# Optimization experiments

Hardware: AMD Instinct MI355X
Metric: run time of the kernel (lower is better)

Reference implementation:

```python
import jax, jax.numpy as jnp
import numpy as np

B, T, D, NH, N, NL, V = 1, 4096, 256, 4, 256, 4, 256
TWO_PI = 2.0 * np.pi
THETA = 2.0 ** 16


def _ln(x):
    # LayerNorm over last dim, no affine, eps=1e-5 (torch default)
    mu = x.mean(-1, keepdims=True)
    var = ((x - mu) ** 2).mean(-1, keepdims=True)
    return (x - mu) * jax.lax.rsqrt(var + 1e-5)


def _rope(phases, v):
    # phases: [T,N] broadcast over [B,nh,T,N]; per-index (interleaved-pair) rotation
    v_rot = jnp.stack((-v[..., 1::2], v[..., ::2]), axis=-1).reshape(v.shape)
    ph = (phases % 1.0) * TWO_PI
    return v * jnp.cos(ph) + v_rot * jnp.sin(ph)


def setup_inputs() -> dict:
    key = jax.random.key(0)
    k0, k1, k2, k3, k4, k5 = jax.random.split(key, 6)
    idx = jax.random.randint(k0, (B, T), 0, V)
    embed = jax.random.normal(k1, (V, D), dtype=jnp.float32) * 0.02
    encoder = jax.random.normal(k2, (NH, D, N), dtype=jnp.float32) * 0.02
    encoder_v = jax.random.normal(k3, (NH, D, N), dtype=jnp.float32) * 0.02
    decoder = jax.random.normal(k4, (NH * N, D), dtype=jnp.float32) * 0.02
    lm_head = jax.random.normal(k5, (D, V), dtype=jnp.float32) * 0.02
    freqs = (1.0 / THETA ** (jnp.arange(N, dtype=jnp.float32) / N)) / TWO_PI  # [N]
    return {"idx": idx, "embed": embed, "encoder": encoder,
            "encoder_v": encoder_v, "decoder": decoder,
            "lm_head": lm_head, "freqs": freqs}


def reference(idx, embed, encoder, encoder_v, decoder, lm_head, freqs):
    r_phases = jnp.arange(T, dtype=jnp.float32)[:, None] * freqs[None, :]  # [T,N]
    x = _ln(embed[idx][:, None])  # [B,1,T,D]
    for _ in range(NL):
        x_sparse = jax.nn.relu(x @ encoder)           # [B,nh,T,N]
        QR = _rope(r_phases, x_sparse)                # [B,nh,T,N]
        scores = jnp.tril(QR @ jnp.swapaxes(QR, -1, -2), k=-1)  # [B,nh,T,T], no softmax
        yKV = _ln(scores @ x)                         # [B,nh,T,D] (V broadcast from [B,1,T,D])
        y_sparse = jax.nn.relu(yKV @ encoder_v)       # [B,nh,T,N]
        xy_sparse = x_sparse * y_sparse               # gated sparse activations
        yMLP = jnp.swapaxes(xy_sparse, 1, 2).reshape(B, 1, T, NH * N) @ decoder  # [B,1,T,D]
        x = _ln(x + _ln(yMLP))
    logits = x.reshape(B, T, D) @ lm_head  # [B,T,V]
    return logits
```

## Files before the change

### kernel.cpp

```cpp
#include <hip/hip_runtime.h>
#include <hip/hip_bf16.h>

#define T   4096
#define D   256
#define NH  4
#define NN  256
#define NL  4
#define VV  256
#define CI  64
#define NC  (T/CI)

typedef short bf16x4 __attribute__((ext_vector_type(4)));
typedef short bf16x8 __attribute__((ext_vector_type(8)));
typedef float f32x4  __attribute__((ext_vector_type(4)));

__device__ __forceinline__ short f2bf(float f) {
    union { float f; unsigned u; } v; v.f = f;
    unsigned r = v.u + 0x7fffu + ((v.u >> 16) & 1u);
    return (short)(r >> 16);
}
__device__ __forceinline__ float bf2f(short s) {
    union { unsigned u; float f; } v; v.u = ((unsigned)(unsigned short)s) << 16;
    return v.f;
}
__device__ __forceinline__ f32x4 mfma16(bf16x8 a, bf16x8 b, f32x4 c) {
    return __builtin_amdgcn_mfma_f32_16x16x32_bf16(a, b, c, 0, 0, 0);
}

__global__ void __launch_bounds__(256) k_wtr(const float* __restrict__ src,
                                             short* __restrict__ dst, int R, int C) {
    int b = blockIdx.z, r0 = blockIdx.x * 16, c0 = blockIdx.y * 16;
    int i = threadIdx.x >> 4, j = threadIdx.x & 15;
    __shared__ float tile[16][17];
    tile[i][j] = src[((size_t)b * R + r0 + i) * C + c0 + j];
    __syncthreads();
    dst[((size_t)b * C + c0 + i) * R + r0 + j] = f2bf(tile[j][i]);
}

__global__ void k_rope(const float* __restrict__ freqs,
                       float* __restrict__ rcos, float* __restrict__ rsin) {
    int t = blockIdx.x, n = threadIdx.x;
    float p = (float)t * freqs[n];
    float fr = p - floorf(p);
    float ang = fr * 6.283185307179586f;
    rcos[(size_t)t * NN + n] = cosf(ang);
    rsin[(size_t)t * NN + n] = sinf(ang);
}

__global__ void __launch_bounds__(256) k_embed(const int* __restrict__ idx,
                                               const float* __restrict__ embed,
                                               short* __restrict__ xT) {
    int t0 = blockIdx.x * 32, tid = threadIdx.x;
    __shared__ float ld[32][257];
    __shared__ int ridx[32];
    __shared__ float mu_s[32], rs_s[32];
    if (tid < 32) ridx[tid] = idx[t0 + tid];
    __syncthreads();
    for (int k = 0; k < 32; k++) ld[k][tid] = embed[(size_t)ridx[k] * D + tid];
    __syncthreads();
    int r = tid >> 3, l8 = tid & 7;
    float s = 0.f, q = 0.f;
    for (int d = l8; d < D; d += 8) { float v = ld[r][d]; s += v; q += v * v; }
#pragma unroll
    for (int m = 1; m < 8; m <<= 1) { s += __shfl_xor(s, m); q += __shfl_xor(q, m); }
    if (l8 == 0) {
        float mu = s * (1.f / D);
        float var = q * (1.f / D) - mu * mu;
        mu_s[r] = mu; rs_s[r] = rsqrtf(fmaxf(var, 0.f) + 1e-5f);
    }
    __syncthreads();
    short vals[32];
#pragma unroll
    for (int rr = 0; rr < 32; rr++) vals[rr] = f2bf((ld[rr][tid] - mu_s[rr]) * rs_s[rr]);
    bf16x8* p = (bf16x8*)(xT + (size_t)tid * T + t0);
#pragma unroll
    for (int u = 0; u < 4; u++) p[u] = *(bf16x8*)&vals[u * 8];
}

__global__ void __launch_bounds__(256) k_tr(const short* __restrict__ src,
                                            short* __restrict__ dst, int R, int C) {
    int z = blockIdx.z;
    int c0 = blockIdx.x * 64, r0 = blockIdx.y * 64;
    int tid = threadIdx.x;
    __shared__ short ld[64][72];
    const short* s = src + (size_t)z * R * C;
    short* d = dst + (size_t)z * R * C;
    {
        int i = tid >> 2, c4 = (tid & 3) * 16;
        const bf16x8* p = (const bf16x8*)(s + (size_t)(r0 + i) * C + c0 + c4);
        bf16x8 v0 = p[0], v1 = p[1];
        int sw = (i & 7) << 3;
        *(bf16x8*)&ld[i][c4 ^ sw] = v0;
        *(bf16x8*)&ld[i][(c4 + 8) ^ sw] = v1;
    }
    __syncthreads();
    {
        int j = tid >> 2, r4 = (tid & 3) * 16;
        short vals[16];
#pragma unroll
        for (int m = 0; m < 16; m++) vals[m] = ld[r4 + m][j ^ ((m & 7) << 3)];
        bf16x8* q = (bf16x8*)(d + (size_t)(c0 + j) * R + r0 + r4);
        q[0] = *(bf16x8*)&vals[0];
        q[1] = *(bf16x8*)&vals[8];
    }
}

__global__ void __launch_bounds__(256) k_encode(const short* __restrict__ x_bf,
                                                const short* __restrict__ encT,
                                                const float* __restrict__ rc,
                                                const float* __restrict__ rs,
                                                short* __restrict__ xs,
                                                short* __restrict__ qr) {
    int h = blockIdx.y, t0 = blockIdx.x * 32;
    int tid = threadIdx.x, w = tid >> 6, l = tid & 63;
    int l15 = l & 15, lk = (l >> 4) * 8, lr4 = (l >> 4) * 4;
    int nstrip = w * 64;
    const short* ebase = encT + ((size_t)h * NN + nstrip + l15) * D + lk;
    const short* xbase = x_bf + (size_t)(t0 + l15) * D + lk;
    f32x4 acc[4][2];
#pragma unroll
    for (int rt = 0; rt < 4; rt++)
#pragma unroll
        for (int tt = 0; tt < 2; tt++) acc[rt][tt] = (f32x4){0.f, 0.f, 0.f, 0.f};
    for (int k0 = 0; k0 < D; k0 += 32) {
        bf16x8 a[4], b[2];
#pragma unroll
        for (int rt = 0; rt < 4; rt++) a[rt] = *(const bf16x8*)(ebase + rt * 16 * D + k0);
#pragma unroll
        for (int tt = 0; tt < 2; tt++) b[tt] = *(const bf16x8*)(xbase + tt * 16 * D + k0);
#pragma unroll
        for (int rt = 0; rt < 4; rt++)
#pragma unroll
            for (int tt = 0; tt < 2; tt++) acc[rt][tt] = mfma16(a[rt], b[tt], acc[rt][tt]);
    }
#pragma unroll
    for (int rt = 0; rt < 4; rt++)
#pragma unroll
        for (int tt = 0; tt < 2; tt++) {
            int t = t0 + tt * 16 + l15;
            int n0 = nstrip + rt * 16 + lr4;
            float v[4], rot[4];
#pragma unroll
            for (int r = 0; r < 4; r++) v[r] = fmaxf(acc[rt][tt][r], 0.f);
            rot[0] = -v[1]; rot[1] = v[0]; rot[2] = -v[3]; rot[3] = v[2];
            bf16x4 xsv;
#pragma unroll
            for (int r = 0; r < 4; r++) xsv[r] = f2bf(v[r]);
            *(bf16x4*)(xs + ((size_t)h * T + t) * NN + n0) = xsv;
            float4 cv = *(const float4*)(rc + (size_t)t * NN + n0);
            float4 sv = *(const float4*)(rs + (size_t)t * NN + n0);
            float cc[4] = {cv.x, cv.y, cv.z, cv.w}, ss[4] = {sv.x, sv.y, sv.z, sv.w};
            bf16x4 qv;
#pragma unroll
            for (int r = 0; r < 4; r++) qv[r] = f2bf(v[r] * cc[r] + rot[r] * ss[r]);
            *(bf16x4*)(qr + ((size_t)h * T + t) * NN + n0) = qv;
        }
}

__global__ void __launch_bounds__(256) k_gram(const short* __restrict__ qrT,
                                              const short* __restrict__ xT,
                                              short* __restrict__ Graw) {
    int h = blockIdx.z, c = blockIdx.y, n0 = blockIdx.x * 64;
    int tid = threadIdx.x, w = tid >> 6, l = tid & 63;
    int l15 = l & 15, lk = (l >> 4) * 8, lr4 = (l >> 4) * 4;
    const short* abase = qrT + ((size_t)h * NN + n0 + w * 16 + l15) * T + c * CI + lk;
    const short* bbase = xT + (size_t)l15 * T + c * CI + lk;
    f32x4 acc[16];
#pragma unroll
    for (int dt = 0; dt < 16; dt++) acc[dt] = (f32x4){0.f, 0.f, 0.f, 0.f};
#pragma unroll
    for (int ki = 0; ki < 2; ki++) {
        int k0 = ki * 32;
        bf16x8 a = *(const bf16x8*)(abase + k0);
#pragma unroll
        for (int dt = 0; dt < 16; dt++) {
            bf16x8 b = *(const bf16x8*)(bbase + (size_t)dt * 16 * T + k0);
            acc[dt] = mfma16(a, b, acc[dt]);
        }
    }
#pragma unroll
    for (int dt = 0; dt < 16; dt++) {
        int d = dt * 16 + l15;
        bf16x4 o;
#pragma unroll
        for (int r = 0; r < 4; r++) o[r] = f2bf(acc[dt][r]);
        *(bf16x4*)(Graw + (((size_t)h * NC + c) * D + d) * NN + n0 + w * 16 + lr4) = o;
    }
}

__global__ void __launch_bounds__(256) k_prefix(const short* __restrict__ Graw,
                                                short* __restrict__ Sp) {
    int pos = (blockIdx.x * 256 + threadIdx.x) * 4;
    int h = pos >> 16;
    int rem = pos & 65535;
    float run[4] = {0.f, 0.f, 0.f, 0.f};
    for (int c = 0; c < NC; c++) {
        size_t ix = ((size_t)h * NC + c) * 65536 + rem;
        bf16x4 g = *(const bf16x4*)(Graw + ix);
        bf16x4 o;
#pragma unroll
        for (int e = 0; e < 4; e++) { o[e] = f2bf(run[e]); run[e] += bf2f(g[e]); }
        *(bf16x4*)(Sp + ix) = o;
    }
}

__global__ void __launch_bounds__(256) k_attn(const short* __restrict__ qr,
                                              const short* __restrict__ xT,
                                              const short* __restrict__ Sp,
                                              const short* __restrict__ encvT,
                                              const short* __restrict__ xs,
                                              short* __restrict__ xy) {
    int h = blockIdx.y, t0 = blockIdx.x * 32;
    int c = t0 >> 6, cl0 = t0 & 63;
    int tid = threadIdx.x, w = tid >> 6, l = tid & 63;
    int l15 = l & 15, lk = (l >> 4) * 8, lr4 = (l >> 4) * 4;
    int ts = w & 1, dh = w >> 1;
    __shared__ short P_lds[32][72];
    __shared__ short ynorm[32 * 256];
    __shared__ float lnb[2][32][2];
    int njt = cl0 ? 4 : 2;
    const short* qa  = qr + ((size_t)h * T + t0 + ts * 16 + l15) * NN + lk;
    const short* qpb = qr + ((size_t)h * T + c * CI + l15) * NN + lk;
    const short* sb  = Sp + (((size_t)h * NC + c) * D + dh * 128 + l15) * NN + lk;
    f32x4 akv[8], ap[4];
#pragma unroll
    for (int dt = 0; dt < 8; dt++) akv[dt] = (f32x4){0.f, 0.f, 0.f, 0.f};
#pragma unroll
    for (int jt = 0; jt < 4; jt++) ap[jt] = (f32x4){0.f, 0.f, 0.f, 0.f};
    for (int k0 = 0; k0 < NN; k0 += 32) {
        bf16x8 a = *(const bf16x8*)(qa + k0);
#pragma unroll
        for (int dt = 0; dt < 8; dt++) {
            bf16x8 bs = *(const bf16x8*)(sb + (size_t)dt * 16 * NN + k0);
            akv[dt] = mfma16(a, bs, akv[dt]);
        }
        if (dh == 0) {
#pragma unroll
            for (int jt = 0; jt < 4; jt++) {
                if (jt < njt) {
                    bf16x8 bp = *(const bf16x8*)(qpb + (size_t)jt * 16 * NN + k0);
                    ap[jt] = mfma16(a, bp, ap[jt]);
                }
            }
        }
    }
    if (dh == 0) {
#pragma unroll
        for (int jt = 0; jt < 4; jt++) {
            if (jt < njt) {
#pragma unroll
                for (int r = 0; r < 4; r++) {
                    int il = ts * 16 + lr4 + r;
                    int jcl = jt * 16 + l15;
                    float pv = (jcl < cl0 + il) ? ap[jt][r] : 0.f;
                    P_lds[il][jcl] = f2bf(pv);
                }
            }
        }
    }
    __syncthreads();
    int nks = cl0 ? 2 : 1;
    for (int ki = 0; ki < nks; ki++) {
        int k0 = ki * 32;
        bf16x8 a = *(const bf16x8*)(&P_lds[ts * 16 + l15][k0 + lk]);
#pragma unroll
        for (int dt = 0; dt < 8; dt++) {
            bf16x8 b = *(const bf16x8*)(xT + (size_t)(dh * 128 + dt * 16 + l15) * T + c * CI + k0 + lk);
            akv[dt] = mfma16(a, b, akv[dt]);
        }
    }
    float s[4], q[4], mu[4], rstd[4];
#pragma unroll
    for (int r = 0; r < 4; r++) { s[r] = 0.f; q[r] = 0.f; }
#pragma unroll
    for (int dt = 0; dt < 8; dt++)
#pragma unroll
        for (int r = 0; r < 4; r++) { float v = akv[dt][r]; s[r] += v; q[r] += v * v; }
#pragma unroll
    for (int m = 1; m < 16; m <<= 1)
#pragma unroll
        for (int r = 0; r < 4; r++) { s[r] += __shfl_xor(s[r], m); q[r] += __shfl_xor(q[r], m); }
    if (l15 == 0) {
#pragma unroll
        for (int r = 0; r < 4; r++) {
            int rl = ts * 16 + lr4 + r;
            lnb[dh][rl][0] = s[r]; lnb[dh][rl][1] = q[r];
        }
    }
    __syncthreads();
#pragma unroll
    for (int r = 0; r < 4; r++) {
        int rl = ts * 16 + lr4 + r;
        float st = lnb[0][rl][0] + lnb[1][rl][0];
        float qt = lnb[0][rl][1] + lnb[1][rl][1];
        float m_ = st * (1.f / D);
        float var = qt * (1.f / D) - m_ * m_;
        mu[r] = m_; rstd[r] = rsqrtf(fmaxf(var, 0.f) + 1e-5f);
    }
#pragma unroll
    for (int dt = 0; dt < 8; dt++)
#pragma unroll
        for (int r = 0; r < 4; r++) {
            int row = ts * 16 + lr4 + r;
            int dcol = dh * 128 + dt * 16 + l15;
            ynorm[row * 256 + (dcol ^ ((row & 7) << 3))] = f2bf((akv[dt][r] - mu[r]) * rstd[r]);
        }
    __syncthreads();
    int nstrip = w * 64;
    f32x4 a2[4][2];
#pragma unroll
    for (int nt = 0; nt < 4; nt++)
#pragma unroll
        for (int tt = 0; tt < 2; tt++) a2[nt][tt] = (f32x4){0.f, 0.f, 0.f, 0.f};
    const short* ev = encvT + ((size_t)h * NN + nstrip + l15) * D + lk;
    for (int k0 = 0; k0 < D; k0 += 32) {
        bf16x8 av[4], bv[2];
#pragma unroll
        for (int nt = 0; nt < 4; nt++) av[nt] = *(const bf16x8*)(ev + nt * 16 * D + k0);
#pragma unroll
        for (int tt = 0; tt < 2; tt++) {
            int row = tt * 16 + l15;
            int col = k0 + lk;
            bv[tt] = *(const bf16x8*)&ynorm[row * 256 + (col ^ ((row & 7) << 3))];
        }
#pragma unroll
        for (int nt = 0; nt < 4; nt++)
#pragma unroll
            for (int tt = 0; tt < 2; tt++) a2[nt][tt] = mfma16(av[nt], bv[tt], a2[nt][tt]);
    }
#pragma unroll
    for (int nt = 0; nt < 4; nt++)
#pragma unroll
        for (int tt = 0; tt < 2; tt++) {
            int n0 = nstrip + nt * 16 + lr4;
            int t = t0 + tt * 16 + l15;
            bf16x4 g = *(const bf16x4*)(xs + ((size_t)h * T + t) * NN + n0);
            bf16x4 o;
#pragma unroll
            for (int r = 0; r < 4; r++) o[r] = f2bf(fmaxf(a2[nt][tt][r], 0.f) * bf2f(g[r]));
            *(bf16x4*)(xy + (size_t)t * (NH * NN) + h * NN + n0) = o;
        }
}

__global__ void __launch_bounds__(256) k_mlp(const short* __restrict__ xy,
                                             const short* __restrict__ decT,
                                             short* __restrict__ xT) {
    int t0 = blockIdx.x * 16;
    int tid = threadIdx.x, w = tid >> 6, l = tid & 63;
    int l15 = l & 15, lk = (l >> 4) * 8, lr4 = (l >> 4) * 4;
    __shared__ float lnb[4][16][2];
    const short* abase = xy + (size_t)(t0 + l15) * (NH * NN) + lk;
    const short* bbase = decT + (size_t)(w * 64 + l15) * (NH * NN) + lk;
    f32x4 acc[4];
#pragma unroll
    for (int dt = 0; dt < 4; dt++) acc[dt] = (f32x4){0.f, 0.f, 0.f, 0.f};
    for (int k0 = 0; k0 < NH * NN; k0 += 32) {
        bf16x8 a = *(const bf16x8*)(abase + k0);
#pragma unroll
        for (int dt = 0; dt < 4; dt++) {
            bf16x8 b = *(const bf16x8*)(bbase + (size_t)dt * 16 * (NH * NN) + k0);
            acc[dt] = mfma16(a, b, acc[dt]);
        }
    }
    float s[4], q[4];
#pragma unroll
    for (int r = 0; r < 4; r++) { s[r] = 0.f; q[r] = 0.f; }
#pragma unroll
    for (int dt = 0; dt < 4; dt++)
#pragma unroll
        for (int r = 0; r < 4; r++) { float v = acc[dt][r]; s[r] += v; q[r] += v * v; }
#pragma unroll
    for (int m = 1; m < 16; m <<= 1)
#pragma unroll
        for (int r = 0; r < 4; r++) { s[r] += __shfl_xor(s[r], m); q[r] += __shfl_xor(q[r], m); }
    if (l15 == 0)
#pragma unroll
        for (int r = 0; r < 4; r++) { lnb[w][lr4 + r][0] = s[r]; lnb[w][lr4 + r][1] = q[r]; }
    __syncthreads();
    float mu1[4], rstd1[4];
#pragma unroll
    for (int r = 0; r < 4; r++) {
        float st = 0.f, qt = 0.f;
#pragma unroll
        for (int ww = 0; ww < 4; ww++) { st += lnb[ww][lr4 + r][0]; qt += lnb[ww][lr4 + r][1]; }
        float m_ = st * (1.f / D);
        float var = qt * (1.f / D) - m_ * m_;
        mu1[r] = m_; rstd1[r] = rsqrtf(fmaxf(var, 0.f) + 1e-5f);
    }
    float z[4][4];
#pragma unroll
    for (int dt = 0; dt < 4; dt++) {
        bf16x4 xo = *(const bf16x4*)(xT + (size_t)(w * 64 + dt * 16 + l15) * T + t0 + lr4);
#pragma unroll
        for (int r = 0; r < 4; r++)
            z[dt][r] = bf2f(xo[r]) + (acc[dt][r] - mu1[r]) * rstd1[r];
    }
#pragma unroll
    for (int r = 0; r < 4; r++) { s[r] = 0.f; q[r] = 0.f; }
#pragma unroll
    for (int dt = 0; dt < 4; dt++)
#pragma unroll
        for (int r = 0; r < 4; r++) { float v = z[dt][r]; s[r] += v; q[r] += v * v; }
#pragma unroll
    for (int m = 1; m < 16; m <<= 1)
#pragma unroll
        for (int r = 0; r < 4; r++) { s[r] += __shfl_xor(s[r], m); q[r] += __shfl_xor(q[r], m); }
    __syncthreads();
    if (l15 == 0)
#pragma unroll
        for (int r = 0; r < 4; r++) { lnb[w][lr4 + r][0] = s[r]; lnb[w][lr4 + r][1] = q[r]; }
    __syncthreads();
#pragma unroll
    for (int r = 0; r < 4; r++) {
        float st = 0.f, qt = 0.f;
#pragma unroll
        for (int ww = 0; ww < 4; ww++) { st += lnb[ww][lr4 + r][0]; qt += lnb[ww][lr4 + r][1]; }
        float m_ = st * (1.f / D);
        float var = qt * (1.f / D) - m_ * m_;
        mu1[r] = m_; rstd1[r] = rsqrtf(fmaxf(var, 0.f) + 1e-5f);
    }
#pragma unroll
    for (int dt = 0; dt < 4; dt++) {
        bf16x4 o;
#pragma unroll
        for (int r = 0; r < 4; r++) o[r] = f2bf((z[dt][r] - mu1[r]) * rstd1[r]);
        *(bf16x4*)(xT + (size_t)(w * 64 + dt * 16 + l15) * T + t0 + lr4) = o;
    }
}

__global__ void __launch_bounds__(256) k_logits(const short* __restrict__ x_bf,
                                                const short* __restrict__ lmhT,
                                                float* __restrict__ out) {
    int t0 = blockIdx.x * 16;
    int tid = threadIdx.x, w = tid >> 6, l = tid & 63;
    int l15 = l & 15, lk = (l >> 4) * 8, lr4 = (l >> 4) * 4;
    const short* ab = lmhT + (size_t)(w * 64 + l15) * D + lk;
    const short* bb = x_bf + (size_t)(t0 + l15) * D + lk;
    f32x4 acc[4];
#pragma unroll
    for (int vt = 0; vt < 4; vt++) acc[vt] = (f32x4){0.f, 0.f, 0.f, 0.f};
    for (int k0 = 0; k0 < D; k0 += 32) {
        bf16x8 b = *(const bf16x8*)(bb + k0);
#pragma unroll
        for (int vt = 0; vt < 4; vt++) {
            bf16x8 a = *(const bf16x8*)(ab + (size_t)vt * 16 * D + k0);
            acc[vt] = mfma16(a, b, acc[vt]);
        }
    }
#pragma unroll
    for (int vt = 0; vt < 4; vt++) {
        int t = t0 + l15;
        int v0 = w * 64 + vt * 16 + lr4;
        *(f32x4*)(out + (size_t)t * VV + v0) = acc[vt];
    }
}

extern "C" void kernel_launch(void* const* d_in, const int* in_sizes, int n_in,
                              void* d_out, int out_size, void* d_ws, size_t ws_size,
                              hipStream_t stream) {
    const int*   idx   = (const int*)d_in[0];
    const float* embed = (const float*)d_in[1];
    const float* enc   = (const float*)d_in[2];
    const float* encv  = (const float*)d_in[3];
    const float* dec   = (const float*)d_in[4];
    const float* lmh   = (const float*)d_in[5];
    const float* freqs = (const float*)d_in[6];
    float* out = (float*)d_out;

    float* rc = (float*)d_ws;
    float* rs = rc + (size_t)T * NN;
    short* xT    = (short*)(rs + (size_t)T * NN);
    short* x_bf  = xT + (size_t)D * T;
    short* xs    = x_bf + (size_t)T * D;
    short* qr    = xs + (size_t)NH * T * NN;
    short* qrT   = qr + (size_t)NH * T * NN;
    short* xy    = qrT + (size_t)NH * NN * T;
    short* Graw  = xy + (size_t)T * NH * NN;
    short* Sp    = Graw + (size_t)NH * NC * D * NN;
    short* encT  = Sp + (size_t)NH * NC * D * NN;
    short* encvT = encT + (size_t)NH * NN * D;
    short* decT  = encvT + (size_t)NH * NN * D;
    short* lmhT  = decT + (size_t)D * NH * NN;

    k_wtr<<<dim3(16, 16, 4), 256, 0, stream>>>(enc,  encT, D, NN);
    k_wtr<<<dim3(16, 16, 4), 256, 0, stream>>>(encv, encvT, D, NN);
    k_wtr<<<dim3(64, 16, 1), 256, 0, stream>>>(dec,  decT, NH * NN, D);
    k_wtr<<<dim3(16, 16, 1), 256, 0, stream>>>(lmh,  lmhT, D, VV);
    k_rope<<<T, 256, 0, stream>>>(freqs, rc, rs);
    k_embed<<<T / 32, 256, 0, stream>>>(idx, embed, xT);
    k_tr<<<dim3(T / 64, D / 64, 1), 256, 0, stream>>>(xT, x_bf, D, T);

    for (int l = 0; l < NL; l++) {
        k_encode<<<dim3(T / 32, NH), 256, 0, stream>>>(x_bf, encT, rc, rs, xs, qr);
        k_tr<<<dim3(NN / 64, T / 64, NH), 256, 0, stream>>>(qr, qrT, T, NN);
        k_gram<<<dim3(NN / 64, NC, NH), 256, 0, stream>>>(qrT, xT, Graw);
        k_prefix<<<256, 256, 0, stream>>>(Graw, Sp);
        k_attn<<<dim3(T / 32, NH), 256, 0, stream>>>(qr, xT, Sp, encvT, xs, xy);
        k_mlp<<<T / 16, 256, 0, stream>>>(xy, decT, xT);
        k_tr<<<dim3(T / 64, D / 64, 1), 256, 0, stream>>>(xT, x_bf, D, T);
    }
    k_logits<<<T / 16, 256, 0, stream>>>(x_bf, lmhT, out);
}
```

Baseline: 611.2 us.

## Double chunk size to 128 and widen attention blocks to 64 rows with 8 waves

```diff
diff --git a/kernel.cpp b/kernel.cpp
--- a/kernel.cpp
+++ b/kernel.cpp
@@ -7,7 +7,7 @@
 #define NN  256
 #define NL  4
 #define VV  256
-#define CI  64
+#define CI  128
 #define NC  (T/CI)
 
 typedef short bf16x4 __attribute__((ext_vector_type(4)));
@@ -163,13 +163,13 @@
     int h = blockIdx.z, c = blockIdx.y, n0 = blockIdx.x * 64;
     int tid = threadIdx.x, w = tid >> 6, l = tid & 63;
     int l15 = l & 15, lk = (l >> 4) * 8, lr4 = (l >> 4) * 4;
-    const short* abase = qrT + ((size_t)h * NN + n0 + w * 16 + l15) * T + c * CI + lk;
-    const short* bbase = xT + (size_t)l15 * T + c * CI + lk;
+    const short* abase = qrT + ((size_t)h * NN + n0 + w * 16 + l15) * T + (size_t)c * CI + lk;
+    const short* bbase = xT + (size_t)l15 * T + (size_t)c * CI + lk;
     f32x4 acc[16];
 #pragma unroll
     for (int dt = 0; dt < 16; dt++) acc[dt] = (f32x4){0.f, 0.f, 0.f, 0.f};
 #pragma unroll
-    for (int ki = 0; ki < 2; ki++) {
+    for (int ki = 0; ki < CI / 32; ki++) {
         int k0 = ki * 32;
         bf16x8 a = *(const bf16x8*)(abase + k0);
 #pragma unroll
@@ -204,29 +204,29 @@
     }
 }
 
-__global__ void __launch_bounds__(256) k_attn(const short* __restrict__ qr,
+__global__ void __launch_bounds__(512) k_attn(const short* __restrict__ qr,
                                               const short* __restrict__ xT,
                                               const short* __restrict__ Sp,
                                               const short* __restrict__ encvT,
                                               const short* __restrict__ xs,
                                               short* __restrict__ xy) {
-    int h = blockIdx.y, t0 = blockIdx.x * 32;
-    int c = t0 >> 6, cl0 = t0 & 63;
+    int h = blockIdx.y, t0 = blockIdx.x * 64;
+    int c = t0 >> 7, cl0 = t0 & 127;
     int tid = threadIdx.x, w = tid >> 6, l = tid & 63;
     int l15 = l & 15, lk = (l >> 4) * 8, lr4 = (l >> 4) * 4;
-    int ts = w & 1, dh = w >> 1;
-    __shared__ short P_lds[32][72];
-    __shared__ short ynorm[32 * 256];
-    __shared__ float lnb[2][32][2];
-    int njt = cl0 ? 4 : 2;
-    const short* qa  = qr + ((size_t)h * T + t0 + ts * 16 + l15) * NN + lk;
-    const short* qpb = qr + ((size_t)h * T + c * CI + l15) * NN + lk;
+    int rt = w & 3, dh = w >> 2;
+    int ntiles = (((cl0 >> 4) + rt) | 1) + 1;
+    __shared__ short P_lds[64][136];
+    __shared__ short ynorm[64 * 256];
+    __shared__ float lnb[2][64][2];
+    const short* qa  = qr + ((size_t)h * T + t0 + rt * 16 + l15) * NN + lk;
+    const short* qpb = qr + ((size_t)h * T + (size_t)c * CI + l15) * NN + lk;
     const short* sb  = Sp + (((size_t)h * NC + c) * D + dh * 128 + l15) * NN + lk;
     f32x4 akv[8], ap[4];
 #pragma unroll
     for (int dt = 0; dt < 8; dt++) akv[dt] = (f32x4){0.f, 0.f, 0.f, 0.f};
 #pragma unroll
-    for (int jt = 0; jt < 4; jt++) ap[jt] = (f32x4){0.f, 0.f, 0.f, 0.f};
+    for (int ji = 0; ji < 4; ji++) ap[ji] = (f32x4){0.f, 0.f, 0.f, 0.f};
     for (int k0 = 0; k0 < NN; k0 += 32) {
         bf16x8 a = *(const bf16x8*)(qa + k0);
 #pragma unroll
@@ -234,39 +234,40 @@
             bf16x8 bs = *(const bf16x8*)(sb + (size_t)dt * 16 * NN + k0);
             akv[dt] = mfma16(a, bs, akv[dt]);
         }
-        if (dh == 0) {
-#pragma unroll
-            for (int jt = 0; jt < 4; jt++) {
-                if (jt < njt) {
-                    bf16x8 bp = *(const bf16x8*)(qpb + (size_t)jt * 16 * NN + k0);
-                    ap[jt] = mfma16(a, bp, ap[jt]);
-                }
+#pragma unroll
+        for (int ji = 0; ji < 4; ji++) {
+            int jt = ji * 2 + dh;
+            if (jt < ntiles) {
+                bf16x8 bp = *(const bf16x8*)(qpb + (size_t)jt * 16 * NN + k0);
+                ap[ji] = mfma16(a, bp, ap[ji]);
             }
         }
     }
-    if (dh == 0) {
-#pragma unroll
-        for (int jt = 0; jt < 4; jt++) {
-            if (jt < njt) {
-#pragma unroll
-                for (int r = 0; r < 4; r++) {
-                    int il = ts * 16 + lr4 + r;
-                    int jcl = jt * 16 + l15;
-                    float pv = (jcl < cl0 + il) ? ap[jt][r] : 0.f;
-                    P_lds[il][jcl] = f2bf(pv);
-                }
+#pragma unroll
+    for (int ji = 0; ji < 4; ji++) {
+        int jt = ji * 2 + dh;
+        if (jt < ntiles) {
+#pragma unroll
+            for (int r = 0; r < 4; r++) {
+                int lrow = rt * 16 + lr4 + r;
+                int jcl  = jt * 16 + l15;
+                float pv = (jcl < cl0 + lrow) ? ap[ji][r] : 0.f;
+                P_lds[lrow][jcl] = f2bf(pv);
             }
         }
     }
     __syncthreads();
-    int nks = cl0 ? 2 : 1;
-    for (int ki = 0; ki < nks; ki++) {
-        int k0 = ki * 32;
-        bf16x8 a = *(const bf16x8*)(&P_lds[ts * 16 + l15][k0 + lk]);
-#pragma unroll
-        for (int dt = 0; dt < 8; dt++) {
-            bf16x8 b = *(const bf16x8*)(xT + (size_t)(dh * 128 + dt * 16 + l15) * T + c * CI + k0 + lk);
-            akv[dt] = mfma16(a, b, akv[dt]);
+    int ksteps = ntiles >> 1;
+#pragma unroll
+    for (int ki = 0; ki < 4; ki++) {
+        if (ki < ksteps) {
+            bf16x8 a = *(const bf16x8*)&P_lds[rt * 16 + l15][ki * 32 + lk];
+#pragma unroll
+            for (int dt = 0; dt < 8; dt++) {
+                bf16x8 b = *(const bf16x8*)(xT + (size_t)(dh * 128 + dt * 16 + l15) * T
+                                            + (size_t)c * CI + ki * 32 + lk);
+                akv[dt] = mfma16(a, b, akv[dt]);
+            }
         }
     }
     float s[4], q[4], mu[4], rstd[4];
@@ -283,16 +284,16 @@
     if (l15 == 0) {
 #pragma unroll
         for (int r = 0; r < 4; r++) {
-            int rl = ts * 16 + lr4 + r;
-            lnb[dh][rl][0] = s[r]; lnb[dh][rl][1] = q[r];
+            int lrow = rt * 16 + lr4 + r;
+            lnb[dh][lrow][0] = s[r]; lnb[dh][lrow][1] = q[r];
         }
     }
     __syncthreads();
 #pragma unroll
     for (int r = 0; r < 4; r++) {
-        int rl = ts * 16 + lr4 + r;
-        float st = lnb[0][rl][0] + lnb[1][rl][0];
-        float qt = lnb[0][rl][1] + lnb[1][rl][1];
+        int lrow = rt * 16 + lr4 + r;
+        float st = lnb[0][lrow][0] + lnb[1][lrow][0];
+        float qt = lnb[0][lrow][1] + lnb[1][lrow][1];
         float m_ = st * (1.f / D);
         float var = qt * (1.f / D) - m_ * m_;
         mu[r] = m_; rstd[r] = rsqrtf(fmaxf(var, 0.f) + 1e-5f);
@@ -301,37 +302,36 @@
     for (int dt = 0; dt < 8; dt++)
 #pragma unroll
         for (int r = 0; r < 4; r++) {
-            int row = ts * 16 + lr4 + r;
+            int lrow = rt * 16 + lr4 + r;
             int dcol = dh * 128 + dt * 16 + l15;
-            ynorm[row * 256 + (dcol ^ ((row & 7) << 3))] = f2bf((akv[dt][r] - mu[r]) * rstd[r]);
-        }
-    __syncthreads();
-    int nstrip = w * 64;
-    f32x4 a2[4][2];
-#pragma unroll
-    for (int nt = 0; nt < 4; nt++)
-#pragma unroll
-        for (int tt = 0; tt < 2; tt++) a2[nt][tt] = (f32x4){0.f, 0.f, 0.f, 0.f};
+            ynorm[lrow * 256 + (dcol ^ ((lrow & 7) << 3))] = f2bf((akv[dt][r] - mu[r]) * rstd[r]);
+        }
+    __syncthreads();
+    int nstrip = w * 32;
+    f32x4 a2[2][4];
+#pragma unroll
+    for (int nt = 0; nt < 2; nt++)
+#pragma unroll
+        for (int tt = 0; tt < 4; tt++) a2[nt][tt] = (f32x4){0.f, 0.f, 0.f, 0.f};
     const short* ev = encvT + ((size_t)h * NN + nstrip + l15) * D + lk;
     for (int k0 = 0; k0 < D; k0 += 32) {
-        bf16x8 av[4], bv[2];
-#pragma unroll
-        for (int nt = 0; nt < 4; nt++) av[nt] = *(const bf16x8*)(ev + nt * 16 * D + k0);
-#pragma unroll
-        for (int tt = 0; tt < 2; tt++) {
+        bf16x8 av[2], bv[4];
+#pragma unroll
+        for (int nt = 0; nt < 2; nt++) av[nt] = *(const bf16x8*)(ev + nt * 16 * D + k0);
+#pragma unroll
+        for (int tt = 0; tt < 4; tt++) {
             int row = tt * 16 + l15;
-            int col = k0 + lk;
-            bv[tt] = *(const bf16x8*)&ynorm[row * 256 + (col ^ ((row & 7) << 3))];
-        }
-#pragma unroll
-        for (int nt = 0; nt < 4; nt++)
-#pragma unroll
-            for (int tt = 0; tt < 2; tt++) a2[nt][tt] = mfma16(av[nt], bv[tt], a2[nt][tt]);
-    }
-#pragma unroll
-    for (int nt = 0; nt < 4; nt++)
-#pragma unroll
-        for (int tt = 0; tt < 2; tt++) {
+            bv[tt] = *(const bf16x8*)&ynorm[row * 256 + ((k0 + lk) ^ ((l15 & 7) << 3))];
+        }
+#pragma unroll
+        for (int nt = 0; nt < 2; nt++)
+#pragma unroll
+            for (int tt = 0; tt < 4; tt++) a2[nt][tt] = mfma16(av[nt], bv[tt], a2[nt][tt]);
+    }
+#pragma unroll
+    for (int nt = 0; nt < 2; nt++)
+#pragma unroll
+        for (int tt = 0; tt < 4; tt++) {
             int n0 = nstrip + nt * 16 + lr4;
             int t = t0 + tt * 16 + l15;
             bf16x4 g = *(const bf16x4*)(xs + ((size_t)h * T + t) * NN + n0);
@@ -495,7 +495,7 @@
         k_tr<<<dim3(NN / 64, T / 64, NH), 256, 0, stream>>>(qr, qrT, T, NN);
         k_gram<<<dim3(NN / 64, NC, NH), 256, 0, stream>>>(qrT, xT, Graw);
         k_prefix<<<256, 256, 0, stream>>>(Graw, Sp);
-        k_attn<<<dim3(T / 32, NH), 256, 0, stream>>>(qr, xT, Sp, encvT, xs, xy);
+        k_attn<<<dim3(T / 64, NH), 512, 0, stream>>>(qr, xT, Sp, encvT, xs, xy);
         k_mlp<<<T / 16, 256, 0, stream>>>(xy, decT, xT);
         k_tr<<<dim3(T / 64, D / 64, 1), 256, 0, stream>>>(xT, x_bf, D, T);
     }
```

New measurement: 584.4 us. 4.4% less time.
